# Optimization experiments

Measured on AMD Instinct MI355X. Metric: run time of the kernel, lower is better.

## Reference

```python
import jax, jax.numpy as jnp
import numpy as np

HORIZON, CITIES = 96, 32

def _rmsnorm(x, w, eps=1e-5):
    return x * jax.lax.rsqrt(jnp.mean(x * x, axis=-1, keepdims=True) + eps) * w

def _mamba_block(h, in_w, conv_w, conv_b, xproj_w, dt_w, dt_b, A_log, Dp):
    d_inner = Dp.shape[0]
    d_state = A_log.shape[-1]
    d_conv = conv_w.shape[-1]
    xz = h @ in_w.T                              # (B,L,2*ED)
    xc, z = jnp.split(xz, 2, axis=-1)
    # depthwise causal conv over time
    xt = xc.transpose(0, 2, 1)                   # (B,ED,L)
    xt = jax.lax.conv_general_dilated(
        xt, conv_w, window_strides=(1,), padding=[(d_conv - 1, 0)],
        feature_group_count=d_inner, dimension_numbers=('NCH', 'OIH', 'NCH'))
    xc = jax.nn.silu(xt.transpose(0, 2, 1) + conv_b)   # (B,L,ED)
    dbc = xc @ xproj_w.T                          # (B,L,dt_rank+2N)
    dt_rank = dt_w.shape[-1]
    delta, Bm, Cm = jnp.split(dbc, [dt_rank, dt_rank + d_state], axis=-1)
    delta = jax.nn.softplus(delta @ dt_w.T + dt_b)     # (B,L,ED)
    A = -jnp.exp(A_log)                                # (ED,N)
    def step(hst, inp):
        dlt, Bt, Ct, ut = inp                     # (B,ED),(B,N),(B,N),(B,ED)
        dA = jnp.exp(dlt[:, :, None] * A)         # (B,ED,N)
        hst = dA * hst + (dlt * ut)[:, :, None] * Bt[:, None, :]
        y = jnp.einsum('ben,bn->be', hst, Ct)
        return hst, y
    bsz = xc.shape[0]
    h0 = jnp.zeros((bsz, d_inner, d_state), xc.dtype)
    xs = (delta.transpose(1, 0, 2), Bm.transpose(1, 0, 2),
          Cm.transpose(1, 0, 2), xc.transpose(1, 0, 2))
    _, ys = jax.lax.scan(step, h0, xs)            # ys: (L,B,ED)
    y = ys.transpose(1, 0, 2) + Dp * xc
    return y * jax.nn.silu(z)

def setup_inputs():
    B, L, IN, D, NL, N, DC, E = 16, 1024, 32, 512, 4, 16, 4, 2
    ED, DR = E * D, (D + 15) // 16
    key = jax.random.key(0)
    ks = jax.random.split(key, 12)
    g = lambda k, s: jax.random.normal(k, s, jnp.float32) * 0.02
    return {
        'x': jax.random.normal(ks[0], (B, IN, L), jnp.float32),
        'embed_w': g(ks[1], (D, IN)),
        'embed_b': jnp.zeros((D,), jnp.float32),
        'norm_w': jnp.ones((NL, D), jnp.float32),
        'in_proj_w': g(ks[2], (NL, 2 * ED, D)),
        'conv_w': g(ks[3], (NL, ED, 1, DC)),
        'conv_b': jnp.zeros((NL, ED), jnp.float32),
        'x_proj_w': g(ks[4], (NL, DR + 2 * N, ED)),
        'dt_proj_w': g(ks[5], (NL, ED, DR)),
        'dt_proj_b': jnp.full((NL, ED), -4.6, jnp.float32) + g(ks[6], (NL, ED)),
        'A_log': jnp.broadcast_to(jnp.log(jnp.arange(1., N + 1, dtype=jnp.float32)), (NL, ED, N)).copy(),
        'D': jnp.ones((NL, ED), jnp.float32),
        'out_proj_w': g(ks[7], (NL, D, ED)),
        'head_w': g(ks[8], (HORIZON * CITIES, D)),
        'head_b': jnp.zeros((HORIZON * CITIES,), jnp.float32),
    }

def reference(x, embed_w, embed_b, norm_w, in_proj_w, conv_w, conv_b,
              x_proj_w, dt_proj_w, dt_proj_b, A_log, D, out_proj_w,
              head_w, head_b):
    h = x.transpose(0, 2, 1) @ embed_w.T + embed_b     # (B,L,d_model)
    for i in range(in_proj_w.shape[0]):
        blk = _mamba_block(_rmsnorm(h, norm_w[i]), in_proj_w[i], conv_w[i],
                           conv_b[i], x_proj_w[i], dt_proj_w[i], dt_proj_b[i],
                           A_log[i], D[i])
        h = h + blk @ out_proj_w[i].T                  # residual block
    y = h[:, -1, :] @ head_w.T + head_b                # (B, horizon*cities)
    return y.reshape(-1, HORIZON, CITIES).transpose(0, 2, 1)  # (B,cities,horizon)
```

## Files before the change

kernel.cpp:

```cpp
#include <hip/hip_runtime.h>
#include <hip/hip_bf16.h>


#define B_ 16
#define L_ 1024
#define D_ 512
#define ED_ 1024
#define N_ 16
#define DR_ 32
#define DC_ 4
#define BL_ (B_ * L_)

typedef __attribute__((ext_vector_type(8))) __bf16 bf16x8;
typedef __attribute__((ext_vector_type(4))) float f32x4;

#define ASYNC_LDS16(G, L)                                                      \
  __builtin_amdgcn_global_load_lds(                                            \
      (const __attribute__((address_space(1))) void*)(G),                      \
      (__attribute__((address_space(3))) void*)(L), 16, 0, 0)

__device__ __forceinline__ float bf2f(unsigned short v) {
  unsigned int u = (unsigned int)v << 16;
  return __builtin_bit_cast(float, u);
}

__global__ __launch_bounds__(256) void embed_kernel(
    const float* __restrict__ x, const float* __restrict__ w,
    const float* __restrict__ bias, float* __restrict__ h) {
  __shared__ float xs[64][36];
  __shared__ float ws[32][513];
  const int tid = threadIdx.x;
  const int b = blockIdx.y, l0 = blockIdx.x * 64;
  for (int f = tid; f < 16384; f += 256) {
    int d = f >> 5, i = f & 31;
    ws[i][d] = w[f];
  }
  for (int f = tid; f < 2048; f += 256) {
    int i = f >> 6, l = f & 63;
    xs[l][i] = x[b * 32768 + i * 1024 + l0 + l];
  }
  const int d0 = tid, d1 = tid + 256;
  __syncthreads();
  float wr0[32], wr1[32];
#pragma unroll
  for (int i = 0; i < 32; ++i) {
    wr0[i] = ws[i][d0];
    wr1[i] = ws[i][d1];
  }
  const float b0 = bias[d0], b1 = bias[d1];
  for (int l = 0; l < 64; ++l) {
    float a0 = b0, a1 = b1;
#pragma unroll
    for (int q = 0; q < 8; ++q) {
      float4 xv = *(float4*)&xs[l][q * 4];
      a0 = fmaf(xv.x, wr0[q * 4], a0);
      a1 = fmaf(xv.x, wr1[q * 4], a1);
      a0 = fmaf(xv.y, wr0[q * 4 + 1], a0);
      a1 = fmaf(xv.y, wr1[q * 4 + 1], a1);
      a0 = fmaf(xv.z, wr0[q * 4 + 2], a0);
      a1 = fmaf(xv.z, wr1[q * 4 + 2], a1);
      a0 = fmaf(xv.w, wr0[q * 4 + 3], a0);
      a1 = fmaf(xv.w, wr1[q * 4 + 3], a1);
    }
    size_t row = (size_t)(b << 10) + l0 + l;
    h[row * 512 + d0] = a0;
    h[row * 512 + d1] = a1;
  }
}

__global__ __launch_bounds__(256) void cvt_bf16_kernel(
    const float* __restrict__ src, __hip_bfloat16* __restrict__ dst, int n4) {
  int i = blockIdx.x * 256 + threadIdx.x;
  if (i < n4) {
    float4 v = *(const float4*)&src[(size_t)i * 4];
    __hip_bfloat16 t4[4] = {__float2bfloat16(v.x), __float2bfloat16(v.y),
                            __float2bfloat16(v.z), __float2bfloat16(v.w)};
    *(ushort4*)&dst[(size_t)i * 4] = *(ushort4*)t4;
  }
}

__global__ __launch_bounds__(256) void transpose_xp_kernel(
    const float* __restrict__ xp, __hip_bfloat16* __restrict__ xpT) {
  int t = blockIdx.x * 256 + threadIdx.x;
  int r = t & 31, k = (t >> 5) & 1023, i = t >> 15;
  xpT[i * 32768 + k * 32 + r] = __float2bfloat16(xp[i * 65536 + r * 1024 + k]);
}

__global__ __launch_bounds__(256) void wcat_tail_kernel(
    const float* __restrict__ xp, __hip_bfloat16* __restrict__ wcat) {
  int t = blockIdx.x * 256 + threadIdx.x;
  int k = t & 1023, row = (t >> 10) & 63, i = t >> 16;
  float v = (row < 32) ? xp[i * 65536 + (32 + row) * 1024 + k] : 0.f;
  wcat[(size_t)i * 1114112 + (size_t)(1024 + row) * 1024 + k] =
      __float2bfloat16(v);
}

__global__ __launch_bounds__(256) void rmsnorm_kernel(
    const float* __restrict__ h, const float* __restrict__ w,
    __hip_bfloat16* __restrict__ hn) {
  const int tid = threadIdx.x;
  const int row = blockIdx.x * 2 + (tid >> 7);
  const int t = tid & 127;
  float4 v = *(const float4*)&h[(size_t)row * 512 + t * 4];
  float ss = v.x * v.x + v.y * v.y + v.z * v.z + v.w * v.w;
#pragma unroll
  for (int o = 32; o; o >>= 1) ss += __shfl_down(ss, o);
  __shared__ float red[2][2];
  if ((tid & 63) == 0) red[tid >> 7][(tid >> 6) & 1] = ss;
  __syncthreads();
  float tot = red[tid >> 7][0] + red[tid >> 7][1];
  float scale = rsqrtf(tot * (1.f / D_) + 1e-5f);
  float4 wv = *(const float4*)&w[t * 4];
  __hip_bfloat16 t4[4] = {__float2bfloat16(v.x * scale * wv.x),
                          __float2bfloat16(v.y * scale * wv.y),
                          __float2bfloat16(v.z * scale * wv.z),
                          __float2bfloat16(v.w * scale * wv.w)};
  *(ushort4*)&hn[(size_t)row * 512 + t * 4] = *(ushort4*)t4;
}

template <int BM, int BN, int EPI>
__global__ __launch_bounds__(256) void gemm_mfma_kernel(
    const __hip_bfloat16* __restrict__ A, int lda,
    const __hip_bfloat16* __restrict__ W, float* __restrict__ C, int ldc,
    __hip_bfloat16* __restrict__ auxb, __hip_bfloat16* __restrict__ auxb2,
    const float* __restrict__ bias, int K) {
  constexpr int FM = BM / 32, FN = BN / 32;
  __shared__ __bf16 As[2][BM * 32];
  __shared__ __bf16 Bs[2][BN * 32];
  const int tid = threadIdx.x;
  const int w = tid >> 6, l = tid & 63;
  const int gx = gridDim.x;
  const int nwg = gx * gridDim.y;
  const int wg = blockIdx.y * gx + blockIdx.x;
  const int q = nwg >> 3, r = nwg & 7;
  const int xcd = wg & 7, pos = wg >> 3;
  const int wgid =
      (xcd < r ? xcd * (q + 1) : r * (q + 1) + (xcd - r) * q) + pos;
  const int m0 = (wgid / gx) * BM, n0 = (wgid % gx) * BN;
  const int wr = w >> 1, wc = w & 1;
  const int lrow = l & 15, lk = (l >> 4) * 8;

  const size_t arow0 = (size_t)(m0 + w * 16 + lrow) * lda + lk;
  const size_t arow1 = (size_t)(m0 + (w + 4) * 16 + lrow) * lda + lk;
  const size_t brow0 = (size_t)(n0 + w * 16 + lrow) * K + lk;
  const size_t brow1 = (size_t)(n0 + (w + 4) * 16 + lrow) * K + lk;

  f32x4 acc[FM][FN];
#pragma unroll
  for (int i = 0; i < FM; ++i)
#pragma unroll
    for (int j = 0; j < FN; ++j) acc[i][j] = (f32x4)0.f;

  auto stage = [&](int bufi, int k0) {
    ASYNC_LDS16(A + arow0 + k0, &As[bufi][w * 512]);
    if constexpr (BM == 128)
      ASYNC_LDS16(A + arow1 + k0, &As[bufi][(w + 4) * 512]);
    ASYNC_LDS16(W + brow0 + k0, &Bs[bufi][w * 512]);
    if constexpr (BN == 128)
      ASYNC_LDS16(W + brow1 + k0, &Bs[bufi][(w + 4) * 512]);
  };

  stage(0, 0);
  int buf = 0;
  for (int k0 = 0; k0 < K; k0 += 32) {
    __syncthreads();
    if (k0 + 32 < K) stage(buf ^ 1, k0 + 32);
    bf16x8 af[FM], bfr[FN];
#pragma unroll
    for (int mi = 0; mi < FM; ++mi)
      af[mi] = *(bf16x8*)&As[buf][(wr * FM + mi) * 512 + l * 8];
#pragma unroll
    for (int ni = 0; ni < FN; ++ni)
      bfr[ni] = *(bf16x8*)&Bs[buf][(wc * FN + ni) * 512 + l * 8];
#pragma unroll
    for (int mi = 0; mi < FM; ++mi)
#pragma unroll
      for (int ni = 0; ni < FN; ++ni)
        acc[mi][ni] = __builtin_amdgcn_mfma_f32_16x16x32_bf16(
            af[mi], bfr[ni], acc[mi][ni], 0, 0, 0);
    buf ^= 1;
  }

#pragma unroll
  for (int mi = 0; mi < FM; ++mi) {
#pragma unroll
    for (int ni = 0; ni < FN; ++ni) {
      int row0 = m0 + (wr * FM + mi) * 16 + (l >> 4) * 4;
      int col = n0 + (wc * FN + ni) * 16 + (l & 15);
#pragma unroll
      for (int r2 = 0; r2 < 4; ++r2) {
        int row = row0 + r2;
        float v = acc[mi][ni][r2];
        if (EPI == 1) {
          C[(size_t)row * ldc + col] += v;
        } else if (EPI == 5) {
          if (col < 1024) {
            auxb[(size_t)row * 1024 + col] = __float2bfloat16(v);
          } else {
            float g = v / (1.f + __expf(-v));
            auxb2[(size_t)row * 1024 + (col - 1024)] = __float2bfloat16(g);
          }
        } else if (EPI == 6) {
          auxb[(size_t)row * ldc + col] = __float2bfloat16(v);
        } else if (EPI == 8) {
          if (col < 1024) {
            v += bias[col];
            v = (v > 20.f) ? v : log1pf(__expf(v));
            auxb[(size_t)row * 1024 + col] = __float2bfloat16(v);
          } else if (col < 1056) {
            C[(size_t)row * 32 + (col - 1024)] = v;
          }
        }
      }
    }
  }
}

__global__ __launch_bounds__(256) void conv_silu_kernel(
    const __hip_bfloat16* __restrict__ xcb, const float* __restrict__ cw,
    const float* __restrict__ cb, __hip_bfloat16* __restrict__ out) {
  int i = blockIdx.x * 256 + threadIdx.x;
  int ed = (i & 127) * 8;
  int bl = i >> 7;
  int l = bl & 1023;
  float4 cwv[8];
#pragma unroll
  for (int e = 0; e < 8; ++e) cwv[e] = *(const float4*)&cw[(ed + e) * 4];
  float ac[8];
  {
    float4 c0 = *(const float4*)&cb[ed];
    float4 c1 = *(const float4*)&cb[ed + 4];
    ac[0] = c0.x; ac[1] = c0.y; ac[2] = c0.z; ac[3] = c0.w;
    ac[4] = c1.x; ac[5] = c1.y; ac[6] = c1.z; ac[7] = c1.w;
  }
#pragma unroll
  for (int j = 0; j < DC_; ++j) {
    if (l - 3 + j >= 0) {
      const __hip_bfloat16* src = &xcb[(size_t)(bl - 3 + j) * 1024 + ed];
      ushort4 a = *(const ushort4*)src;
      ushort4 b = *(const ushort4*)(src + 4);
      unsigned short xv[8] = {a.x, a.y, a.z, a.w, b.x, b.y, b.z, b.w};
#pragma unroll
      for (int e = 0; e < 8; ++e)
        ac[e] = fmaf(bf2f(xv[e]), ((const float*)&cwv[e])[j], ac[e]);
    }
  }
  __hip_bfloat16 t8[8];
#pragma unroll
  for (int e = 0; e < 8; ++e) {
    float v = ac[e] / (1.f + __expf(-ac[e]));
    t8[e] = __float2bfloat16(v);
  }
  *(ushort4*)&out[(size_t)bl * 1024 + ed] = *(ushort4*)&t8[0];
  *(ushort4*)&out[(size_t)bl * 1024 + ed + 4] = *(ushort4*)&t8[4];
}

__global__ __launch_bounds__(256) void scan_p1_kernel(
    const unsigned short* __restrict__ dlt, const float* __restrict__ dbc,
    const unsigned short* __restrict__ xc, const float* __restrict__ A_log,
    float* __restrict__ S, float* __restrict__ totd) {
  const int tid = threadIdx.x;
  const int ed = blockIdx.x * 256 + tid;
  const int c = blockIdx.y, b = blockIdx.z;
  const size_t row0 = ((size_t)b << 10) + c * 64;
  __shared__ float sB[64][16];
  {
    const int w = tid >> 6, l = tid & 63;
    ASYNC_LDS16(&dbc[(row0 + w * 16 + (l >> 2)) * 32 + (l & 3) * 4],
                &sB[w * 16][0]);
  }
  float An[16], h[16];
#pragma unroll
  for (int n = 0; n < 16; n += 4) {
    float4 a = *(const float4*)&A_log[ed * 16 + n];
    An[n] = -__expf(a.x);
    An[n + 1] = -__expf(a.y);
    An[n + 2] = -__expf(a.z);
    An[n + 3] = -__expf(a.w);
    h[n] = h[n + 1] = h[n + 2] = h[n + 3] = 0.f;
  }
  float cd = 0.f;
  size_t gi = row0 * 1024 + ed;
  __syncthreads();
  unsigned short nd = dlt[gi], nu = xc[gi];
#pragma unroll 4
  for (int t = 0; t < 64; ++t) {
    float dv = bf2f(nd), u = bf2f(nu);
    if (t < 63) {
      nd = dlt[gi + 1024];
      nu = xc[gi + 1024];
    }
    float du = dv * u;
    cd += dv;
    float Bv[16];
    *(float4*)&Bv[0] = *(float4*)&sB[t][0];
    *(float4*)&Bv[4] = *(float4*)&sB[t][4];
    *(float4*)&Bv[8] = *(float4*)&sB[t][8];
    *(float4*)&Bv[12] = *(float4*)&sB[t][12];
#pragma unroll
    for (int n = 0; n < 16; ++n)
      h[n] = fmaf(__expf(dv * An[n]), h[n], du * Bv[n]);
    gi += 1024;
  }
  const size_t so = (((size_t)b * 16 + c) * 1024 + ed) * 16;
  *(float4*)&S[so] = make_float4(h[0], h[1], h[2], h[3]);
  *(float4*)&S[so + 4] = make_float4(h[4], h[5], h[6], h[7]);
  *(float4*)&S[so + 8] = make_float4(h[8], h[9], h[10], h[11]);
  *(float4*)&S[so + 12] = make_float4(h[12], h[13], h[14], h[15]);
  totd[((size_t)b * 16 + c) * 1024 + ed] = cd;
}

__global__ __launch_bounds__(256) void scan_p2_kernel(
    const float* __restrict__ S, const float* __restrict__ totd,
    const float* __restrict__ A_log, float* __restrict__ HP) {
  int t = blockIdx.x * 256 + threadIdx.x;
  int n = t & 15, ed = (t >> 4) & 1023;
  int b = t >> 14;
  float An = -__expf(A_log[ed * 16 + n]);
  float H = 0.f;
#pragma unroll
  for (int c = 0; c < 16; ++c) {
    size_t i = ((size_t)b * 16 + c) * 1024 + ed;
    HP[i * 16 + n] = H;
    H = fmaf(__expf(An * totd[i]), H, S[i * 16 + n]);
  }
}

__global__ __launch_bounds__(256) void scan_p3_kernel(
    const unsigned short* __restrict__ dlt, const float* __restrict__ dbc,
    const unsigned short* __restrict__ xc, const float* __restrict__ A_log,
    const float* __restrict__ Dp, const float* __restrict__ HP,
    unsigned short* __restrict__ yg) {
  const int tid = threadIdx.x;
  const int ed = blockIdx.x * 256 + tid;
  const int c = blockIdx.y, b = blockIdx.z;
  const size_t row0 = ((size_t)b << 10) + c * 64;
  __shared__ float sBC[64][32];
  {
    const int w = tid >> 6, l = tid & 63;
    ASYNC_LDS16(&dbc[(row0 + w * 16 + (l >> 3)) * 32 + (l & 7) * 4],
                &sBC[w * 16][0]);
    ASYNC_LDS16(&dbc[(row0 + w * 16 + 8 + (l >> 3)) * 32 + (l & 7) * 4],
                &sBC[w * 16 + 8][0]);
  }
  float An[16], h[16];
  const size_t ho = (((size_t)b * 16 + c) * 1024 + ed) * 16;
#pragma unroll
  for (int n = 0; n < 16; n += 4) {
    float4 a = *(const float4*)&A_log[ed * 16 + n];
    An[n] = -__expf(a.x);
    An[n + 1] = -__expf(a.y);
    An[n + 2] = -__expf(a.z);
    An[n + 3] = -__expf(a.w);
    *(float4*)&h[n] = *(const float4*)&HP[ho + n];
  }
  const float Dv = Dp[ed];
  size_t gi = row0 * 1024 + ed;
  __syncthreads();
  unsigned short nd = dlt[gi], nu = xc[gi], ng = yg[gi];
#pragma unroll 2
  for (int t = 0; t < 64; ++t) {
    float dv = bf2f(nd), u = bf2f(nu), g = bf2f(ng);
    if (t < 63) {
      nd = dlt[gi + 1024];
      nu = xc[gi + 1024];
      ng = yg[gi + 1024];
    }
    float du = dv * u;
    float y = Dv * u;
    float Bv[16], Cv[16];
    *(float4*)&Bv[0] = *(float4*)&sBC[t][0];
    *(float4*)&Bv[4] = *(float4*)&sBC[t][4];
    *(float4*)&Bv[8] = *(float4*)&sBC[t][8];
    *(float4*)&Bv[12] = *(float4*)&sBC[t][12];
    *(float4*)&Cv[0] = *(float4*)&sBC[t][16];
    *(float4*)&Cv[4] = *(float4*)&sBC[t][20];
    *(float4*)&Cv[8] = *(float4*)&sBC[t][24];
    *(float4*)&Cv[12] = *(float4*)&sBC[t][28];
#pragma unroll
    for (int n = 0; n < 16; ++n) {
      h[n] = fmaf(__expf(dv * An[n]), h[n], du * Bv[n]);
      y = fmaf(h[n], Cv[n], y);
    }
    __hip_bfloat16 yb = __float2bfloat16(y * g);
    yg[gi] = *(unsigned short*)&yb;
    gi += 1024;
  }
}

__global__ __launch_bounds__(256) void head_kernel(
    const float* __restrict__ h, const float* __restrict__ hw,
    const float* __restrict__ hb, float* __restrict__ out) {
  int hc = blockIdx.x * 256 + threadIdx.x;
  int b = blockIdx.y;
  __shared__ float hs[D_];
  for (int d = threadIdx.x; d < D_; d += 256)
    hs[d] = h[((size_t)(b << 10) + 1023) * D_ + d];
  __syncthreads();
  float s = hb[hc];
#pragma unroll 16
  for (int d = 0; d < D_; d += 4) {
    float4 wv = *(const float4*)&hw[(size_t)hc * D_ + d];
    s = fmaf(hs[d], wv.x, s);
    s = fmaf(hs[d + 1], wv.y, s);
    s = fmaf(hs[d + 2], wv.z, s);
    s = fmaf(hs[d + 3], wv.w, s);
  }
  int t = hc >> 5, c = hc & 31;
  out[(size_t)b * 3072 + c * 96 + t] = s;
}

extern "C" void kernel_launch(void* const* d_in, const int* in_sizes, int n_in,
                              void* d_out, int out_size, void* d_ws,
                              size_t ws_size, hipStream_t stream) {
  const float* x = (const float*)d_in[0];
  const float* embed_w = (const float*)d_in[1];
  const float* embed_b = (const float*)d_in[2];
  const float* norm_w = (const float*)d_in[3];
  const float* in_proj_w = (const float*)d_in[4];
  const float* conv_w = (const float*)d_in[5];
  const float* conv_b = (const float*)d_in[6];
  const float* x_proj_w = (const float*)d_in[7];
  const float* dt_proj_w = (const float*)d_in[8];
  const float* dt_proj_b = (const float*)d_in[9];
  const float* A_log = (const float*)d_in[10];
  const float* Dp = (const float*)d_in[11];
  const float* out_proj_w = (const float*)d_in[12];
  const float* head_w = (const float*)d_in[13];
  const float* head_b = (const float*)d_in[14];
  float* out = (float*)d_out;

  const size_t fixed0 = 33554432ull + 8388608ull + 4194304ull + 262144ull +
                        262144ull + 8912896ull;
  auto need = [&](int cbx) {
    return fixed0 + (size_t)cbx * (2ull * 1048576 + 65536) +
           (size_t)cbx * 1024 * 7296;
  };
  int cb = 16;
  while (cb > 1 && need(cb) > ws_size) cb >>= 1;
  if (need(cb) > ws_size) return;
  const int Mc = cb * 1024;
  const int nchunks = 16 / cb;

  char* p = (char*)d_ws;
  float* h = (float*)p;                         p += 33554432ull;
  __hip_bfloat16* wbi = (__hip_bfloat16*)p;     p += 8388608ull;
  __hip_bfloat16* wbo = (__hip_bfloat16*)p;     p += 4194304ull;
  __hip_bfloat16* wxpT = (__hip_bfloat16*)p;    p += 262144ull;
  __hip_bfloat16* wdtbf = (__hip_bfloat16*)p;   p += 262144ull;
  __hip_bfloat16* wcat = (__hip_bfloat16*)p;    p += 8912896ull;
  float* S = (float*)p;                         p += (size_t)cb * 1048576;
  float* HP = (float*)p;                        p += (size_t)cb * 1048576;
  float* totd = (float*)p;                      p += (size_t)cb * 65536;
  __hip_bfloat16* hn = (__hip_bfloat16*)p;      p += (size_t)Mc * 1024;
  __hip_bfloat16* buf1 = (__hip_bfloat16*)p;    p += (size_t)Mc * 2048;
  __hip_bfloat16* buf2 = (__hip_bfloat16*)p;    p += (size_t)Mc * 2048;
  __hip_bfloat16* xcsbf = (__hip_bfloat16*)p;   p += (size_t)Mc * 2048;
  float* dbc = (float*)p;

  cvt_bf16_kernel<<<4096, 256, 0, stream>>>(in_proj_w, wbi, 1048576);
  cvt_bf16_kernel<<<2048, 256, 0, stream>>>(out_proj_w, wbo, 524288);
  cvt_bf16_kernel<<<128, 256, 0, stream>>>(dt_proj_w, wdtbf, 32768);
  transpose_xp_kernel<<<512, 256, 0, stream>>>(x_proj_w, wxpT);
  wcat_tail_kernel<<<1024, 256, 0, stream>>>(x_proj_w, wcat);
  for (int i = 0; i < 4; ++i)
    gemm_mfma_kernel<128, 128, 6><<<dim3(8, 8), 256, 0, stream>>>(
        wdtbf + (size_t)i * 32768, 32, wxpT + (size_t)i * 32768, nullptr, 1024,
        wcat + (size_t)i * 1114112, nullptr, nullptr, 32);
  embed_kernel<<<dim3(16, 16), 256, 0, stream>>>(x, embed_w, embed_b, h);

  for (int i = 0; i < 4; ++i) {
    const float* Ai = A_log + (size_t)i * ED_ * N_;
    for (int ch = 0; ch < nchunks; ++ch) {
      float* hc = h + (size_t)ch * Mc * D_;
      rmsnorm_kernel<<<Mc / 2, 256, 0, stream>>>(hc, norm_w + i * D_, hn);
      gemm_mfma_kernel<128, 128, 5><<<dim3(16, Mc / 128), 256, 0, stream>>>(
          hn, D_, wbi + (size_t)i * 1048576, nullptr, 0, buf1, buf2, nullptr,
          D_);
      conv_silu_kernel<<<Mc / 2, 256, 0, stream>>>(
          buf1, conv_w + i * ED_ * DC_, conv_b + i * ED_, xcsbf);
      gemm_mfma_kernel<128, 64, 8><<<dim3(17, Mc / 128), 256, 0, stream>>>(
          xcsbf, ED_, wcat + (size_t)i * 1114112, dbc, 0, buf1, nullptr,
          dt_proj_b + i * ED_, ED_);
      scan_p1_kernel<<<dim3(4, 16, cb), 256, 0, stream>>>(
          (const unsigned short*)buf1, dbc, (const unsigned short*)xcsbf, Ai,
          S, totd);
      scan_p2_kernel<<<cb * 64, 256, 0, stream>>>(S, totd, Ai, HP);
      scan_p3_kernel<<<dim3(4, 16, cb), 256, 0, stream>>>(
          (const unsigned short*)buf1, dbc, (const unsigned short*)xcsbf, Ai,
          Dp + i * ED_, HP, (unsigned short*)buf2);
      gemm_mfma_kernel<128, 128, 1><<<dim3(4, Mc / 128), 256, 0, stream>>>(
          buf2, ED_, wbo + (size_t)i * 524288, hc, D_, nullptr, nullptr,
          nullptr, ED_);
    }
  }

  head_kernel<<<dim3(12, B_), 256, 0, stream>>>(h, head_w, head_b, out);
}
```

Before: 1.997 ms.

## Enlarge GEMM tiles to 256-row blocks with 512 threads and K=64 steps

Replaces the 128x128/128x64 MFMA GEMM with a 256xBN tile kernel using 8 waves and a K step of 64, for the in_proj, x_proj/dt and out_proj GEMMs. The larger tiles raise arithmetic intensity and halve the number of barriers per K. The x_proj concatenated weight is padded from 1088 to 1280 rows so it fits 256-wide N tiles, which means extra zero columns get computed. Larger shared memory use and more accumulator registers per thread may lower occupancy, and the grids get smaller.

```diff
diff --git a/kernel.cpp b/kernel.cpp
--- a/kernel.cpp
+++ b/kernel.cpp
@@ -89,9 +89,9 @@
 __global__ __launch_bounds__(256) void wcat_tail_kernel(
     const float* __restrict__ xp, __hip_bfloat16* __restrict__ wcat) {
   int t = blockIdx.x * 256 + threadIdx.x;
-  int k = t & 1023, row = (t >> 10) & 63, i = t >> 16;
+  int k = t & 1023, row = (t >> 10) & 255, i = t >> 18;
   float v = (row < 32) ? xp[i * 65536 + (32 + row) * 1024 + k] : 0.f;
-  wcat[(size_t)i * 1114112 + (size_t)(1024 + row) * 1024 + k] =
+  wcat[(size_t)i * 1310720 + (size_t)(1024 + row) * 1024 + k] =
       __float2bfloat16(v);
 }
 
@@ -118,17 +118,79 @@
   *(ushort4*)&hn[(size_t)row * 512 + t * 4] = *(ushort4*)t4;
 }
 
-template <int BM, int BN, int EPI>
 __global__ __launch_bounds__(256) void gemm_mfma_kernel(
+    const __hip_bfloat16* __restrict__ A, int lda,
+    const __hip_bfloat16* __restrict__ W, __hip_bfloat16* __restrict__ auxb,
+    int ldc, int K) {
+  __shared__ __bf16 As[2][4096];
+  __shared__ __bf16 Bs[2][4096];
+  const int tid = threadIdx.x;
+  const int w = tid >> 6, l = tid & 63;
+  const int m0 = blockIdx.y * 128, n0 = blockIdx.x * 128;
+  const int wr = w >> 1, wc = w & 1;
+  const int lrow = l & 15, lk = (l >> 4) * 8;
+  const size_t arow0 = (size_t)(m0 + w * 16 + lrow) * lda + lk;
+  const size_t arow1 = (size_t)(m0 + (w + 4) * 16 + lrow) * lda + lk;
+  const size_t brow0 = (size_t)(n0 + w * 16 + lrow) * K + lk;
+  const size_t brow1 = (size_t)(n0 + (w + 4) * 16 + lrow) * K + lk;
+
+  f32x4 acc[4][4];
+#pragma unroll
+  for (int i = 0; i < 4; ++i)
+#pragma unroll
+    for (int j = 0; j < 4; ++j) acc[i][j] = (f32x4)0.f;
+
+  auto stage = [&](int bufi, int k0) {
+    ASYNC_LDS16(A + arow0 + k0, &As[bufi][w * 512]);
+    ASYNC_LDS16(A + arow1 + k0, &As[bufi][(w + 4) * 512]);
+    ASYNC_LDS16(W + brow0 + k0, &Bs[bufi][w * 512]);
+    ASYNC_LDS16(W + brow1 + k0, &Bs[bufi][(w + 4) * 512]);
+  };
+
+  stage(0, 0);
+  int buf = 0;
+  for (int k0 = 0; k0 < K; k0 += 32) {
+    __syncthreads();
+    if (k0 + 32 < K) stage(buf ^ 1, k0 + 32);
+    bf16x8 af[4], bfr[4];
+#pragma unroll
+    for (int mi = 0; mi < 4; ++mi)
+      af[mi] = *(bf16x8*)&As[buf][(wr * 4 + mi) * 512 + l * 8];
+#pragma unroll
+    for (int ni = 0; ni < 4; ++ni)
+      bfr[ni] = *(bf16x8*)&Bs[buf][(wc * 4 + ni) * 512 + l * 8];
+#pragma unroll
+    for (int mi = 0; mi < 4; ++mi)
+#pragma unroll
+      for (int ni = 0; ni < 4; ++ni)
+        acc[mi][ni] = __builtin_amdgcn_mfma_f32_16x16x32_bf16(
+            af[mi], bfr[ni], acc[mi][ni], 0, 0, 0);
+    buf ^= 1;
+  }
+#pragma unroll
+  for (int mi = 0; mi < 4; ++mi)
+#pragma unroll
+    for (int ni = 0; ni < 4; ++ni) {
+      int row0 = m0 + (wr * 4 + mi) * 16 + (l >> 4) * 4;
+      int col = n0 + (wc * 4 + ni) * 16 + (l & 15);
+#pragma unroll
+      for (int r2 = 0; r2 < 4; ++r2)
+        auxb[(size_t)(row0 + r2) * ldc + col] = __float2bfloat16(acc[mi][ni][r2]);
+    }
+}
+
+template <int BN, int EPI>
+__global__ __launch_bounds__(512) void gemm256_kernel(
     const __hip_bfloat16* __restrict__ A, int lda,
     const __hip_bfloat16* __restrict__ W, float* __restrict__ C, int ldc,
     __hip_bfloat16* __restrict__ auxb, __hip_bfloat16* __restrict__ auxb2,
     const float* __restrict__ bias, int K) {
-  constexpr int FM = BM / 32, FN = BN / 32;
-  __shared__ __bf16 As[2][BM * 32];
-  __shared__ __bf16 Bs[2][BN * 32];
+  constexpr int FN = BN / 64;
+  __shared__ __bf16 As[2][256 * 64];
+  __shared__ __bf16 Bs[2][BN * 64];
   const int tid = threadIdx.x;
   const int w = tid >> 6, l = tid & 63;
+  const int wm = w >> 2, wn = w & 3;
   const int gx = gridDim.x;
   const int nwg = gx * gridDim.y;
   const int wg = blockIdx.y * gx + blockIdx.x;
@@ -136,57 +198,66 @@
   const int xcd = wg & 7, pos = wg >> 3;
   const int wgid =
       (xcd < r ? xcd * (q + 1) : r * (q + 1) + (xcd - r) * q) + pos;
-  const int m0 = (wgid / gx) * BM, n0 = (wgid % gx) * BN;
-  const int wr = w >> 1, wc = w & 1;
+  const int m0 = (wgid / gx) * 256, n0 = (wgid % gx) * BN;
   const int lrow = l & 15, lk = (l >> 4) * 8;
 
-  const size_t arow0 = (size_t)(m0 + w * 16 + lrow) * lda + lk;
-  const size_t arow1 = (size_t)(m0 + (w + 4) * 16 + lrow) * lda + lk;
-  const size_t brow0 = (size_t)(n0 + w * 16 + lrow) * K + lk;
-  const size_t brow1 = (size_t)(n0 + (w + 4) * 16 + lrow) * K + lk;
-
-  f32x4 acc[FM][FN];
-#pragma unroll
-  for (int i = 0; i < FM; ++i)
-#pragma unroll
-    for (int j = 0; j < FN; ++j) acc[i][j] = (f32x4)0.f;
+  unsigned int aoff[4], boff[FN];
+#pragma unroll
+  for (int i = 0; i < 4; ++i) {
+    int s = w * 4 + i;
+    aoff[i] = (unsigned)(m0 + (s >> 1) * 16 + lrow) * lda + (s & 1) * 32 + lk;
+  }
+#pragma unroll
+  for (int i = 0; i < FN; ++i) {
+    int s = w * FN + i;
+    boff[i] = (unsigned)(n0 + (s >> 1) * 16 + lrow) * K + (s & 1) * 32 + lk;
+  }
+
+  f32x4 acc[8][FN];
+#pragma unroll
+  for (int mi = 0; mi < 8; ++mi)
+#pragma unroll
+    for (int ni = 0; ni < FN; ++ni) acc[mi][ni] = (f32x4)0.f;
 
   auto stage = [&](int bufi, int k0) {
-    ASYNC_LDS16(A + arow0 + k0, &As[bufi][w * 512]);
-    if constexpr (BM == 128)
-      ASYNC_LDS16(A + arow1 + k0, &As[bufi][(w + 4) * 512]);
-    ASYNC_LDS16(W + brow0 + k0, &Bs[bufi][w * 512]);
-    if constexpr (BN == 128)
-      ASYNC_LDS16(W + brow1 + k0, &Bs[bufi][(w + 4) * 512]);
+#pragma unroll
+    for (int i = 0; i < 4; ++i)
+      ASYNC_LDS16(A + aoff[i] + k0, &As[bufi][(w * 4 + i) * 512]);
+#pragma unroll
+    for (int i = 0; i < FN; ++i)
+      ASYNC_LDS16(W + boff[i] + k0, &Bs[bufi][(w * FN + i) * 512]);
   };
 
   stage(0, 0);
   int buf = 0;
-  for (int k0 = 0; k0 < K; k0 += 32) {
+  for (int k0 = 0; k0 < K; k0 += 64) {
     __syncthreads();
-    if (k0 + 32 < K) stage(buf ^ 1, k0 + 32);
-    bf16x8 af[FM], bfr[FN];
-#pragma unroll
-    for (int mi = 0; mi < FM; ++mi)
-      af[mi] = *(bf16x8*)&As[buf][(wr * FM + mi) * 512 + l * 8];
-#pragma unroll
-    for (int ni = 0; ni < FN; ++ni)
-      bfr[ni] = *(bf16x8*)&Bs[buf][(wc * FN + ni) * 512 + l * 8];
-#pragma unroll
-    for (int mi = 0; mi < FM; ++mi)
+    if (k0 + 64 < K) stage(buf ^ 1, k0 + 64);
+#pragma unroll
+    for (int kk = 0; kk < 2; ++kk) {
+      bf16x8 bfr[FN];
 #pragma unroll
       for (int ni = 0; ni < FN; ++ni)
-        acc[mi][ni] = __builtin_amdgcn_mfma_f32_16x16x32_bf16(
-            af[mi], bfr[ni], acc[mi][ni], 0, 0, 0);
+        bfr[ni] =
+            *(bf16x8*)&Bs[buf][(((wn * FN + ni) << 1) + kk) * 512 + l * 8];
+#pragma unroll
+      for (int mi = 0; mi < 8; ++mi) {
+        bf16x8 af = *(bf16x8*)&As[buf][(((wm * 8 + mi) << 1) + kk) * 512 + l * 8];
+#pragma unroll
+        for (int ni = 0; ni < FN; ++ni)
+          acc[mi][ni] = __builtin_amdgcn_mfma_f32_16x16x32_bf16(
+              af, bfr[ni], acc[mi][ni], 0, 0, 0);
+      }
+    }
     buf ^= 1;
   }
 
 #pragma unroll
-  for (int mi = 0; mi < FM; ++mi) {
+  for (int mi = 0; mi < 8; ++mi) {
 #pragma unroll
     for (int ni = 0; ni < FN; ++ni) {
-      int row0 = m0 + (wr * FM + mi) * 16 + (l >> 4) * 4;
-      int col = n0 + (wc * FN + ni) * 16 + (l & 15);
+      int row0 = m0 + wm * 128 + mi * 16 + (l >> 4) * 4;
+      int col = n0 + wn * (FN * 16) + ni * 16 + (l & 15);
 #pragma unroll
       for (int r2 = 0; r2 < 4; ++r2) {
         int row = row0 + r2;
@@ -200,8 +271,6 @@
             float g = v / (1.f + __expf(-v));
             auxb2[(size_t)row * 1024 + (col - 1024)] = __float2bfloat16(g);
           }
-        } else if (EPI == 6) {
-          auxb[(size_t)row * ldc + col] = __float2bfloat16(v);
         } else if (EPI == 8) {
           if (col < 1024) {
             v += bias[col];
@@ -431,7 +500,7 @@
   float* out = (float*)d_out;
 
   const size_t fixed0 = 33554432ull + 8388608ull + 4194304ull + 262144ull +
-                        262144ull + 8912896ull;
+                        262144ull + 10485760ull;
   auto need = [&](int cbx) {
     return fixed0 + (size_t)cbx * (2ull * 1048576 + 65536) +
            (size_t)cbx * 1024 * 7296;
@@ -448,7 +517,7 @@
   __hip_bfloat16* wbo = (__hip_bfloat16*)p;     p += 4194304ull;
   __hip_bfloat16* wxpT = (__hip_bfloat16*)p;    p += 262144ull;
   __hip_bfloat16* wdtbf = (__hip_bfloat16*)p;   p += 262144ull;
-  __hip_bfloat16* wcat = (__hip_bfloat16*)p;    p += 8912896ull;
+  __hip_bfloat16* wcat = (__hip_bfloat16*)p;    p += 10485760ull;
   float* S = (float*)p;                         p += (size_t)cb * 1048576;
   float* HP = (float*)p;                        p += (size_t)cb * 1048576;
   float* totd = (float*)p;                      p += (size_t)cb * 65536;
@@ -462,11 +531,11 @@
   cvt_bf16_kernel<<<2048, 256, 0, stream>>>(out_proj_w, wbo, 524288);
   cvt_bf16_kernel<<<128, 256, 0, stream>>>(dt_proj_w, wdtbf, 32768);
   transpose_xp_kernel<<<512, 256, 0, stream>>>(x_proj_w, wxpT);
-  wcat_tail_kernel<<<1024, 256, 0, stream>>>(x_proj_w, wcat);
+  wcat_tail_kernel<<<4096, 256, 0, stream>>>(x_proj_w, wcat);
   for (int i = 0; i < 4; ++i)
-    gemm_mfma_kernel<128, 128, 6><<<dim3(8, 8), 256, 0, stream>>>(
-        wdtbf + (size_t)i * 32768, 32, wxpT + (size_t)i * 32768, nullptr, 1024,
-        wcat + (size_t)i * 1114112, nullptr, nullptr, 32);
+    gemm_mfma_kernel<<<dim3(8, 8), 256, 0, stream>>>(
+        wdtbf + (size_t)i * 32768, 32, wxpT + (size_t)i * 32768,
+        wcat + (size_t)i * 1310720, 1024, 32);
   embed_kernel<<<dim3(16, 16), 256, 0, stream>>>(x, embed_w, embed_b, h);
 
   for (int i = 0; i < 4; ++i) {
@@ -474,13 +543,13 @@
     for (int ch = 0; ch < nchunks; ++ch) {
       float* hc = h + (size_t)ch * Mc * D_;
       rmsnorm_kernel<<<Mc / 2, 256, 0, stream>>>(hc, norm_w + i * D_, hn);
-      gemm_mfma_kernel<128, 128, 5><<<dim3(16, Mc / 128), 256, 0, stream>>>(
+      gemm256_kernel<256, 5><<<dim3(8, Mc / 256), 512, 0, stream>>>(
           hn, D_, wbi + (size_t)i * 1048576, nullptr, 0, buf1, buf2, nullptr,
           D_);
       conv_silu_kernel<<<Mc / 2, 256, 0, stream>>>(
           buf1, conv_w + i * ED_ * DC_, conv_b + i * ED_, xcsbf);
-      gemm_mfma_kernel<128, 64, 8><<<dim3(17, Mc / 128), 256, 0, stream>>>(
-          xcsbf, ED_, wcat + (size_t)i * 1114112, dbc, 0, buf1, nullptr,
+      gemm256_kernel<256, 8><<<dim3(5, Mc / 256), 512, 0, stream>>>(
+          xcsbf, ED_, wcat + (size_t)i * 1310720, dbc, 0, buf1, nullptr,
           dt_proj_b + i * ED_, ED_);
       scan_p1_kernel<<<dim3(4, 16, cb), 256, 0, stream>>>(
           (const unsigned short*)buf1, dbc, (const unsigned short*)xcsbf, Ai,
@@ -489,7 +558,7 @@
       scan_p3_kernel<<<dim3(4, 16, cb), 256, 0, stream>>>(
           (const unsigned short*)buf1, dbc, (const unsigned short*)xcsbf, Ai,
           Dp + i * ED_, HP, (unsigned short*)buf2);
-      gemm_mfma_kernel<128, 128, 1><<<dim3(4, Mc / 128), 256, 0, stream>>>(
+      gemm256_kernel<128, 1><<<dim3(4, Mc / 256), 512, 0, stream>>>(
           buf2, ED_, wbo + (size_t)i * 524288, hc, D_, nullptr, nullptr,
           nullptr, ED_);
     }
```

Measured after the change: 2.276 ms. 1.14x slower.
